# Performance work log

Measured on AMD Instinct MI355X. Metric: run time of the kernel, lower is better.

Reference implementation:

```python
import jax, jax.numpy as jnp
import numpy as np

NUM_MAIN_SEQ_ATOMS = 12   # backbone atoms per RNA residue
NUM_NEIGHBOUR = 30
EMBEDDING_DIM = 32
EPS = 1e-5
BIG_DIST = 1000000.0


def setup_inputs() -> dict:
    key = jax.random.key(0)
    k1, k2, k3 = jax.random.split(key, 3)
    B, L, A = 2, 256, NUM_MAIN_SEQ_ATOMS
    coords = jax.random.normal(k1, (B, L, A, 3), dtype=jnp.float32) * 10.0
    mask = jax.random.randint(k2, (B, L), 0, 2).astype(jnp.int32)
    emb_table = jax.random.normal(k3, (NUM_MAIN_SEQ_ATOMS, EMBEDDING_DIM), dtype=jnp.float32)
    scale = jnp.ones((1, 1, EMBEDDING_DIM), dtype=jnp.float32)
    shift = jnp.zeros((1, 1, EMBEDDING_DIM), dtype=jnp.float32)
    return {"coords": coords, "mask": mask, "emb_table": emb_table,
            "scale": scale, "shift": shift}


def _graph_norm(features, m, scale, shift):
    # features: (B,N,E); m: (B,N) float {0,1}
    mm = m[:, :, None]                                   # (B,N,1)
    masked = features * mm
    cnt = jnp.maximum(mm.sum(axis=1, keepdims=True), 1.0)  # (B,1,1)
    mean = masked.sum(axis=1, keepdims=True) / cnt
    var = ((masked - mean) ** 2).sum(axis=1, keepdims=True) / cnt
    std = jnp.sqrt(var + EPS)
    out = ((features - mean) / std) * scale + shift
    return out * mm


def reference(coords, mask, emb_table, scale, shift):
    B, L, A, _ = coords.shape
    N = L * A
    atom_coords = coords.reshape(B, N, 3)
    atom_mask = jnp.repeat(mask, A, axis=1)              # (B,N) int
    m = atom_mask.astype(coords.dtype)

    # ---- encoder: cyclic atom-type embedding + graph norm ----
    atom_types = jnp.arange(N) % A                       # (N,)
    emb = emb_table[atom_types][None] * m[:, :, None]    # (B,N,E)
    encode = _graph_norm(emb, m, scale, shift)

    # ---- kNN graph: O(N^2) pairwise distances + masked top-k ----
    d = atom_coords[:, None, :, :] - atom_coords[:, :, None, :]  # (B,N,N,3)
    dist = jnp.sqrt((d ** 2).sum(-1) + 1e-6)             # (B,N,N)
    m2 = m[:, None, :] * m[:, :, None]                   # (B,N,N)
    dist = dist * m2 + (1.0 - m2) * BIG_DIST

    k = min(NUM_NEIGHBOUR, N)
    neg_d, edge_idx = jax.lax.top_k(-dist, k)            # smallest-k
    dist_neighbors = -neg_d                              # (B,N,k)

    pad = (atom_mask == 0)[:, :, None]                   # (B,N,1)
    edge_idx = jnp.where(pad, 0, edge_idx)
    dist_neighbors = jnp.where(pad, BIG_DIST, dist_neighbors)
    return atom_coords, atom_mask, encode, dist_neighbors, edge_idx
```

## Files before the change

kernel.cpp:

```cpp
#include <hip/hip_runtime.h>
#include <math.h>

#define NA   12
#define NL   256
#define NN   3072
#define NB   2
#define ED   32
#define KNB  30
#define BIGD 1000000.0f

#define OFF_COORDS 0
#define OFF_MASK   18432
#define OFF_ENC    24576
#define OFF_DIST   221184
#define OFF_IDX    405504

#define WS_C4_BYTE_OFF 512
#define WS_NEEDED (WS_C4_BYTE_OFF + (size_t)NB * NN * 16)

#define KEYVAL 0xFFFFF000u
#define KEYIDX 0x00000FFFu
#define MASKED_D2 1e12f

static __device__ __forceinline__ unsigned umin32(unsigned a, unsigned b) {
    return a < b ? a : b;
}

__global__ __launch_bounds__(256) void prep_kernel(const float* __restrict__ coords,
                                                   const int* __restrict__ mask,
                                                   const float* __restrict__ emb,
                                                   const float* __restrict__ scale,
                                                   const float* __restrict__ shift,
                                                   float* __restrict__ out,
                                                   float4* __restrict__ c4pack) {
    int idx  = blockIdx.x * 256 + threadIdx.x;
    int lane = threadIdx.x & 63;
    int b = idx / (NN * ED);

    const int4* m4 = (const int4*)(mask + b * NL);
    int4 mv = m4[lane];
    float S = (float)(mv.x + mv.y + mv.z + mv.w);
#pragma unroll
    for (int m = 1; m < 64; m <<= 1) S += __shfl_xor(S, m);

    int c = idx & (ED - 1);
    float e[NA];
    float colsum = 0.f;
#pragma unroll
    for (int a = 0; a < NA; ++a) { e[a] = emb[a * ED + c]; colsum += e[a]; }
    float cnt  = fmaxf(12.0f * S, 1.0f);
    float mean = S * colsum / cnt;
    float acc  = 0.f;
#pragma unroll
    for (int a = 0; a < NA; ++a) { float dd = e[a] - mean; acc += dd * dd; }
    float var  = (S * acc + ((float)NN - 12.0f * S) * mean * mean) / cnt;
    float rstd = 1.0f / sqrtf(var + 1e-5f);

    int n  = (idx >> 5) % NN;
    int mi = mask[b * NL + n / NA];
    float v = 0.f;
    if (mi) {
        float en = emb[(n % NA) * ED + c];
        v = (en - mean) * rstd * scale[c] + shift[c];
    }
    out[OFF_ENC + idx] = v;

    if (idx < NB * NN * 3) {
        out[OFF_COORDS + idx] = coords[idx];
    }
    if (idx < NB * NN) {
        int bb = idx / NN, nn = idx - bb * NN;
        float m = (float)mask[bb * NL + nn / NA];
        out[OFF_MASK + idx] = m;
        if (c4pack) {
            float4 p;
            p.x = coords[idx * 3 + 0];
            p.y = coords[idx * 3 + 1];
            p.z = coords[idx * 3 + 2];
            p.w = m;
            c4pack[idx] = p;
        }
    }
}


#define DPP_MIN_STEP(CTRL)                                                        \
    {                                                                             \
        int t_ = __builtin_amdgcn_update_dpp(v_, v_, (CTRL), 0xf, 0xf, false);    \
        v_ = (int)umin32((unsigned)v_, (unsigned)t_);                             \
    }

#define TREE8(A0,A1,A2,A3,A4,A5,A6,A7) \
    umin32(umin32(umin32((A0),(A1)), umin32((A2),(A3))), \
           umin32(umin32((A4),(A5)), umin32((A6),(A7))))

#define REMOVE_RESCAN(G)                                                          \
    {                                                                             \
        _Pragma("unroll")                                                         \
        for (int u = 0; u < 8; ++u) {                                             \
            const int t = (G) * 8 + u;                                            \
            k[t] = (k[t] == wkey) ? 0xFFFFFFFFu : k[t];                           \
        }                                                                         \
        gm[(G)] = TREE8(k[(G)*8+0],k[(G)*8+1],k[(G)*8+2],k[(G)*8+3],              \
                        k[(G)*8+4],k[(G)*8+5],k[(G)*8+6],k[(G)*8+7]);             \
    }

template <bool PACKED>
__global__ __launch_bounds__(256, 2) void topk_kernel(const float4* __restrict__ c4,
                                                      const float* __restrict__ coords,
                                                      const int* __restrict__ mask,
                                                      float* __restrict__ out) {
    int lane = threadIdx.x & 63;
    int row  = blockIdx.x * 4 + (threadIdx.x >> 6);
    int b = (row >= NN) ? 1 : 0;
    int i = row - b * NN;

    float qx, qy, qz, qw;
    if (PACKED) {
        float4 q4 = c4[b * NN + i];
        qx = q4.x; qy = q4.y; qz = q4.z; qw = q4.w;
    } else {
        const float* cb = coords + (size_t)b * NN * 3;
        qx = cb[i * 3 + 0]; qy = cb[i * 3 + 1]; qz = cb[i * 3 + 2];
        qw = (float)mask[b * NL + i / NA];
    }
    if (qw == 0.f) {
        if (lane < KNB) {
            out[OFF_DIST + (size_t)row * KNB + lane] = BIGD;
            out[OFF_IDX  + (size_t)row * KNB + lane] = 0.f;
        }
        return;
    }

    unsigned k[48];
    unsigned gm[6];

#pragma unroll
    for (int t = 0; t < 48; ++t) {
        int j = t * 64 + lane;
        float x, y, z, w;
        if (PACKED) {
            float4 v = c4[b * NN + j];
            x = v.x; y = v.y; z = v.z; w = v.w;
        } else {
            const float* cb = coords + (size_t)b * NN * 3;
            int r = (j * 43691) >> 19;
            w = (float)mask[b * NL + r];
            x = cb[j * 3 + 0]; y = cb[j * 3 + 1]; z = cb[j * 3 + 2];
        }
        float dx = x - qx, dy = y - qy, dz = z - qz;
        float s = dx * dx + dy * dy + dz * dz + 1e-6f;
        s = (w != 0.f) ? s : MASKED_D2;
        k[t] = (__float_as_uint(s) & KEYVAL) | (unsigned)j;
    }
#pragma unroll
    for (int g = 0; g < 6; ++g)
        gm[g] = TREE8(k[g*8+0],k[g*8+1],k[g*8+2],k[g*8+3],
                      k[g*8+4],k[g*8+5],k[g*8+6],k[g*8+7]);

    unsigned cur = umin32(umin32(umin32(gm[0], gm[1]), umin32(gm[2], gm[3])),
                          umin32(gm[4], gm[5]));
    unsigned rkey = 0u;

    for (int it = 0; it < KNB; ++it) {
        int v_ = (int)cur;
        DPP_MIN_STEP(0xB1)
        DPP_MIN_STEP(0x4E)
        DPP_MIN_STEP(0x141)
        DPP_MIN_STEP(0x140)
        unsigned r0  = (unsigned)__builtin_amdgcn_readlane(v_, 0);
        unsigned r16 = (unsigned)__builtin_amdgcn_readlane(v_, 16);
        unsigned r32 = (unsigned)__builtin_amdgcn_readlane(v_, 32);
        unsigned r48 = (unsigned)__builtin_amdgcn_readlane(v_, 48);
        unsigned wkey = umin32(umin32(r0, r16), umin32(r32, r48));
        rkey = (lane == it) ? wkey : rkey;

        int wg = (int)((wkey & KEYIDX) >> 9);
        switch (wg) {
            case 0: REMOVE_RESCAN(0); break;
            case 1: REMOVE_RESCAN(1); break;
            case 2: REMOVE_RESCAN(2); break;
            case 3: REMOVE_RESCAN(3); break;
            case 4: REMOVE_RESCAN(4); break;
            default: REMOVE_RESCAN(5); break;
        }
        cur = umin32(umin32(umin32(gm[0], gm[1]), umin32(gm[2], gm[3])),
                     umin32(gm[4], gm[5]));
    }

    if (lane < KNB) {
        float d2 = __uint_as_float(rkey & KEYVAL);
        out[OFF_DIST + (size_t)row * KNB + lane] = sqrtf(d2);
        out[OFF_IDX  + (size_t)row * KNB + lane] = (float)(rkey & KEYIDX);
    }
}

extern "C" void kernel_launch(void* const* d_in, const int* in_sizes, int n_in,
                              void* d_out, int out_size, void* d_ws, size_t ws_size,
                              hipStream_t stream) {
    const float* coords = (const float*)d_in[0];
    const int*   mask   = (const int*)d_in[1];
    const float* emb    = (const float*)d_in[2];
    const float* scale  = (const float*)d_in[3];
    const float* shift  = (const float*)d_in[4];
    float* out = (float*)d_out;

    bool packed = (ws_size >= WS_NEEDED);
    float4* c4 = packed ? (float4*)((char*)d_ws + WS_C4_BYTE_OFF) : nullptr;

    prep_kernel<<<(NB * NN * ED) / 256, 256, 0, stream>>>(
        coords, mask, emb, scale, shift, out, c4);
    if (packed) {
        topk_kernel<true><<<(NB * NN) / 4, 256, 0, stream>>>(c4, coords, mask, out);
    } else {
        topk_kernel<false><<<(NB * NN) / 4, 256, 0, stream>>>(nullptr, coords, mask, out);
    }
}
```

Measured before the change: 86.87 us.

## Fuse prep and top-k kernels into one launch with LDS-staged coordinates

Merges the encoder/graph-norm prep kernel and the kNN top-k kernel into a single kernel. Each 512-thread block stages the full batch's packed coords and mask (float4 per atom, 48KB) into shared memory, then each wave handles one query row, reading candidate points from LDS instead of global memory. This removes one launch and the workspace round trip. The cost is that every block reloads all 3072 points, and the large LDS footprint limits how many blocks fit per CU.

Result: no change. 87.61 us (+0.9%).

```diff
diff --git a/kernel.cpp b/kernel.cpp
--- a/kernel.cpp
+++ b/kernel.cpp
@@ -15,9 +15,6 @@
 #define OFF_DIST   221184
 #define OFF_IDX    405504
 
-#define WS_C4_BYTE_OFF 512
-#define WS_NEEDED (WS_C4_BYTE_OFF + (size_t)NB * NN * 16)
-
 #define KEYVAL 0xFFFFF000u
 #define KEYIDX 0x00000FFFu
 #define MASKED_D2 1e12f
@@ -25,64 +22,6 @@
 static __device__ __forceinline__ unsigned umin32(unsigned a, unsigned b) {
     return a < b ? a : b;
 }
-
-__global__ __launch_bounds__(256) void prep_kernel(const float* __restrict__ coords,
-                                                   const int* __restrict__ mask,
-                                                   const float* __restrict__ emb,
-                                                   const float* __restrict__ scale,
-                                                   const float* __restrict__ shift,
-                                                   float* __restrict__ out,
-                                                   float4* __restrict__ c4pack) {
-    int idx  = blockIdx.x * 256 + threadIdx.x;
-    int lane = threadIdx.x & 63;
-    int b = idx / (NN * ED);
-
-    const int4* m4 = (const int4*)(mask + b * NL);
-    int4 mv = m4[lane];
-    float S = (float)(mv.x + mv.y + mv.z + mv.w);
-#pragma unroll
-    for (int m = 1; m < 64; m <<= 1) S += __shfl_xor(S, m);
-
-    int c = idx & (ED - 1);
-    float e[NA];
-    float colsum = 0.f;
-#pragma unroll
-    for (int a = 0; a < NA; ++a) { e[a] = emb[a * ED + c]; colsum += e[a]; }
-    float cnt  = fmaxf(12.0f * S, 1.0f);
-    float mean = S * colsum / cnt;
-    float acc  = 0.f;
-#pragma unroll
-    for (int a = 0; a < NA; ++a) { float dd = e[a] - mean; acc += dd * dd; }
-    float var  = (S * acc + ((float)NN - 12.0f * S) * mean * mean) / cnt;
-    float rstd = 1.0f / sqrtf(var + 1e-5f);
-
-    int n  = (idx >> 5) % NN;
-    int mi = mask[b * NL + n / NA];
-    float v = 0.f;
-    if (mi) {
-        float en = emb[(n % NA) * ED + c];
-        v = (en - mean) * rstd * scale[c] + shift[c];
-    }
-    out[OFF_ENC + idx] = v;
-
-    if (idx < NB * NN * 3) {
-        out[OFF_COORDS + idx] = coords[idx];
-    }
-    if (idx < NB * NN) {
-        int bb = idx / NN, nn = idx - bb * NN;
-        float m = (float)mask[bb * NL + nn / NA];
-        out[OFF_MASK + idx] = m;
-        if (c4pack) {
-            float4 p;
-            p.x = coords[idx * 3 + 0];
-            p.y = coords[idx * 3 + 1];
-            p.z = coords[idx * 3 + 2];
-            p.w = m;
-            c4pack[idx] = p;
-        }
-    }
-}
-
 
 #define DPP_MIN_STEP(CTRL)                                                        \
     {                                                                             \
@@ -105,93 +44,142 @@
                         k[(G)*8+4],k[(G)*8+5],k[(G)*8+6],k[(G)*8+7]);             \
     }
 
-template <bool PACKED>
-__global__ __launch_bounds__(256, 2) void topk_kernel(const float4* __restrict__ c4,
-                                                      const float* __restrict__ coords,
-                                                      const int* __restrict__ mask,
-                                                      float* __restrict__ out) {
-    int lane = threadIdx.x & 63;
-    int row  = blockIdx.x * 4 + (threadIdx.x >> 6);
-    int b = (row >= NN) ? 1 : 0;
-    int i = row - b * NN;
+__global__ __launch_bounds__(512, 4) void fused_kernel(const float* __restrict__ coords,
+                                                       const int* __restrict__ mask,
+                                                       const float* __restrict__ emb,
+                                                       const float* __restrict__ scale,
+                                                       const float* __restrict__ shift,
+                                                       float* __restrict__ out) {
+    __shared__ float4 sc4[NN];
 
-    float qx, qy, qz, qw;
-    if (PACKED) {
-        float4 q4 = c4[b * NN + i];
-        qx = q4.x; qy = q4.y; qz = q4.z; qw = q4.w;
+    int tid  = threadIdx.x;
+    int lane = tid & 63;
+    int wave = tid >> 6;
+    int b    = (int)(blockIdx.x) / 384;
+    int rblk = (int)(blockIdx.x) - b * 384;
+    const float* cb = coords + (size_t)b * NN * 3;
+    const int*   mb = mask + b * NL;
+
+#pragma unroll
+    for (int s = 0; s < 6; ++s) {
+        int e = tid + s * 512;
+        int r = (e * 43691) >> 19;
+        float4 p;
+        p.x = cb[e * 3 + 0];
+        p.y = cb[e * 3 + 1];
+        p.z = cb[e * 3 + 2];
+        p.w = (float)mb[r];
+        sc4[e] = p;
+    }
+    __syncthreads();
+
+    int i   = rblk * 8 + wave;
+    int row = b * NN + i;
+    float4 q = sc4[i];
+
+    if (q.w != 0.f) {
+        unsigned k[48];
+        unsigned gm[6];
+
+#pragma unroll
+        for (int t = 0; t < 48; ++t) {
+            int j = t * 64 + lane;
+            float4 v = sc4[j];
+            float dx = v.x - q.x, dy = v.y - q.y, dz = v.z - q.z;
+            float s = dx * dx + dy * dy + dz * dz + 1e-6f;
+            s = (v.w != 0.f) ? s : MASKED_D2;
+            k[t] = (__float_as_uint(s) & KEYVAL) | (unsigned)j;
+        }
+#pragma unroll
+        for (int g = 0; g < 6; ++g)
+            gm[g] = TREE8(k[g*8+0],k[g*8+1],k[g*8+2],k[g*8+3],
+                          k[g*8+4],k[g*8+5],k[g*8+6],k[g*8+7]);
+
+        unsigned cur = umin32(umin32(umin32(gm[0], gm[1]), umin32(gm[2], gm[3])),
+                              umin32(gm[4], gm[5]));
+        unsigned rkey = 0u;
+
+        for (int it = 0; it < KNB; ++it) {
+            int v_ = (int)cur;
+            DPP_MIN_STEP(0xB1)
+            DPP_MIN_STEP(0x4E)
+            DPP_MIN_STEP(0x141)
+            DPP_MIN_STEP(0x140)
+            unsigned r0  = (unsigned)__builtin_amdgcn_readlane(v_, 0);
+            unsigned r16 = (unsigned)__builtin_amdgcn_readlane(v_, 16);
+            unsigned r32 = (unsigned)__builtin_amdgcn_readlane(v_, 32);
+            unsigned r48 = (unsigned)__builtin_amdgcn_readlane(v_, 48);
+            unsigned wkey = umin32(umin32(r0, r16), umin32(r32, r48));
+            rkey = (lane == it) ? wkey : rkey;
+
+            int wg = (int)((wkey & KEYIDX) >> 9);
+            switch (wg) {
+                case 0: REMOVE_RESCAN(0); break;
+                case 1: REMOVE_RESCAN(1); break;
+                case 2: REMOVE_RESCAN(2); break;
+                case 3: REMOVE_RESCAN(3); break;
+                case 4: REMOVE_RESCAN(4); break;
+                default: REMOVE_RESCAN(5); break;
+            }
+            cur = umin32(umin32(umin32(gm[0], gm[1]), umin32(gm[2], gm[3])),
+                         umin32(gm[4], gm[5]));
+        }
+
+        if (lane < KNB) {
+            float d2 = __uint_as_float(rkey & KEYVAL);
+            out[OFF_DIST + (size_t)row * KNB + lane] = sqrtf(d2);
+            out[OFF_IDX  + (size_t)row * KNB + lane] = (float)(rkey & KEYIDX);
+        }
     } else {
-        const float* cb = coords + (size_t)b * NN * 3;
-        qx = cb[i * 3 + 0]; qy = cb[i * 3 + 1]; qz = cb[i * 3 + 2];
-        qw = (float)mask[b * NL + i / NA];
-    }
-    if (qw == 0.f) {
         if (lane < KNB) {
             out[OFF_DIST + (size_t)row * KNB + lane] = BIGD;
             out[OFF_IDX  + (size_t)row * KNB + lane] = 0.f;
         }
-        return;
     }
 
-    unsigned k[48];
-    unsigned gm[6];
+    int gidx = (int)blockIdx.x * 512 + tid;
 
+    if (gidx < NB * NN * ED) {
+        int bb = (gidx >> 5) >= NN ? 1 : 0;
+        const int4* m4 = (const int4*)(mask + bb * NL);
+        int4 mv = m4[lane];
+        float S = (float)(mv.x + mv.y + mv.z + mv.w);
 #pragma unroll
-    for (int t = 0; t < 48; ++t) {
-        int j = t * 64 + lane;
-        float x, y, z, w;
-        if (PACKED) {
-            float4 v = c4[b * NN + j];
-            x = v.x; y = v.y; z = v.z; w = v.w;
-        } else {
-            const float* cb = coords + (size_t)b * NN * 3;
-            int r = (j * 43691) >> 19;
-            w = (float)mask[b * NL + r];
-            x = cb[j * 3 + 0]; y = cb[j * 3 + 1]; z = cb[j * 3 + 2];
+        for (int m = 1; m < 64; m <<= 1) S += __shfl_xor(S, m);
+
+        int c = gidx & (ED - 1);
+        float e[NA];
+        float colsum = 0.f;
+#pragma unroll
+        for (int a = 0; a < NA; ++a) { e[a] = emb[a * ED + c]; colsum += e[a]; }
+        float cnt  = fmaxf(12.0f * S, 1.0f);
+        float mean = S * colsum / cnt;
+        float acc  = 0.f;
+#pragma unroll
+        for (int a = 0; a < NA; ++a) { float dd = e[a] - mean; acc += dd * dd; }
+        float var  = (S * acc + ((float)NN - 12.0f * S) * mean * mean) / cnt;
+        float rstd = 1.0f / sqrtf(var + 1e-5f);
+
+        int n  = (gidx >> 5) - bb * NN;
+        int nr = (n * 43691) >> 19;
+        int mi = mask[bb * NL + nr];
+        float v = 0.f;
+        if (mi) {
+            float en = emb[(n - nr * NA) * ED + c];
+            v = (en - mean) * rstd * scale[c] + shift[c];
         }
-        float dx = x - qx, dy = y - qy, dz = z - qz;
-        float s = dx * dx + dy * dy + dz * dz + 1e-6f;
-        s = (w != 0.f) ? s : MASKED_D2;
-        k[t] = (__float_as_uint(s) & KEYVAL) | (unsigned)j;
-    }
-#pragma unroll
-    for (int g = 0; g < 6; ++g)
-        gm[g] = TREE8(k[g*8+0],k[g*8+1],k[g*8+2],k[g*8+3],
-                      k[g*8+4],k[g*8+5],k[g*8+6],k[g*8+7]);
-
-    unsigned cur = umin32(umin32(umin32(gm[0], gm[1]), umin32(gm[2], gm[3])),
-                          umin32(gm[4], gm[5]));
-    unsigned rkey = 0u;
-
-    for (int it = 0; it < KNB; ++it) {
-        int v_ = (int)cur;
-        DPP_MIN_STEP(0xB1)
-        DPP_MIN_STEP(0x4E)
-        DPP_MIN_STEP(0x141)
-        DPP_MIN_STEP(0x140)
-        unsigned r0  = (unsigned)__builtin_amdgcn_readlane(v_, 0);
-        unsigned r16 = (unsigned)__builtin_amdgcn_readlane(v_, 16);
-        unsigned r32 = (unsigned)__builtin_amdgcn_readlane(v_, 32);
-        unsigned r48 = (unsigned)__builtin_amdgcn_readlane(v_, 48);
-        unsigned wkey = umin32(umin32(r0, r16), umin32(r32, r48));
-        rkey = (lane == it) ? wkey : rkey;
-
-        int wg = (int)((wkey & KEYIDX) >> 9);
-        switch (wg) {
-            case 0: REMOVE_RESCAN(0); break;
-            case 1: REMOVE_RESCAN(1); break;
-            case 2: REMOVE_RESCAN(2); break;
-            case 3: REMOVE_RESCAN(3); break;
-            case 4: REMOVE_RESCAN(4); break;
-            default: REMOVE_RESCAN(5); break;
-        }
-        cur = umin32(umin32(umin32(gm[0], gm[1]), umin32(gm[2], gm[3])),
-                     umin32(gm[4], gm[5]));
+        out[OFF_ENC + gidx] = v;
     }
 
-    if (lane < KNB) {
-        float d2 = __uint_as_float(rkey & KEYVAL);
-        out[OFF_DIST + (size_t)row * KNB + lane] = sqrtf(d2);
-        out[OFF_IDX  + (size_t)row * KNB + lane] = (float)(rkey & KEYIDX);
+    if (gidx < NB * NN * 3) {
+        out[OFF_COORDS + gidx] = coords[gidx];
+    }
+
+    if (gidx < NB * NN) {
+        int bb = gidx >= NN ? 1 : 0;
+        int nn = gidx - bb * NN;
+        int nr = (nn * 43691) >> 19;
+        out[OFF_MASK + gidx] = (float)mask[bb * NL + nr];
     }
 }
 
@@ -205,14 +193,5 @@
     const float* shift  = (const float*)d_in[4];
     float* out = (float*)d_out;
 
-    bool packed = (ws_size >= WS_NEEDED);
-    float4* c4 = packed ? (float4*)((char*)d_ws + WS_C4_BYTE_OFF) : nullptr;
-
-    prep_kernel<<<(NB * NN * ED) / 256, 256, 0, stream>>>(
-        coords, mask, emb, scale, shift, out, c4);
-    if (packed) {
-        topk_kernel<true><<<(NB * NN) / 4, 256, 0, stream>>>(c4, coords, mask, out);
-    } else {
-        topk_kernel<false><<<(NB * NN) / 4, 256, 0, stream>>>(nullptr, coords, mask, out);
-    }
+    fused_kernel<<<NB * (NN / 8), 512, 0, stream>>>(coords, mask, emb, scale, shift, out);
 }
```
